# Optimization experiments

Measured on AMD Instinct MI355X. Metric: run time of the kernel, lower is better.

## Reference

```python
import jax, jax.numpy as jnp
import numpy as np

EPS = 1e-12  # torch F.normalize eps


def setup_inputs() -> dict:
    key = jax.random.key(0)
    k1, k2, k3, k4, k5 = jax.random.split(key, 5)
    N, C, H, W = 32, 512, 32, 32
    E = 1024   # expansion * dim
    G = 8      # group
    D = E // G # 128, per-group channel dim
    K = 64     # num_clusters
    x = jax.random.normal(k1, (N, C, H, W), dtype=jnp.float32)
    W1 = jax.random.normal(k2, (E, C), dtype=jnp.float32) / np.sqrt(C)
    W2 = jax.random.normal(k3, (G, E), dtype=jnp.float32) / np.sqrt(E)
    Wc = jax.random.normal(k4, (K, D), dtype=jnp.float32) / np.sqrt(D)
    centroids = jax.random.uniform(k5, (K, D), dtype=jnp.float32)
    return {"x": x, "W1": W1, "W2": W2, "Wc": Wc, "centroids": centroids}


def reference(x, W1, W2, Wc, centroids):
    # x: [N, C, H, W]; W1: [E, C]; W2: [G, E]; Wc: [K, D]; centroids: [K, D]
    N, C, H, W = x.shape
    E = W1.shape[0]
    G = W2.shape[0]
    K, D = Wc.shape
    P = H * W
    # descriptor-wise L2 normalization over channel dim
    norm = jnp.linalg.norm(x, axis=1, keepdims=True)
    x = x / jnp.maximum(norm, EPS)
    # linear1 on channels: [N, E, P]
    xe = jnp.einsum('ncp,ec->nep', x.reshape(N, C, P), W1)
    # grouped features: [N, G, D, P]
    xg = xe.reshape(N, G, D, P)
    # attention gate: sigmoid(linear2)  -> [N, G, P]
    att = jax.nn.sigmoid(jnp.einsum('nep,ge->ngp', xe, W2))
    # 1x1 conv = per-pixel matmul with cluster weights -> [N, G, K, P]
    soft_assign = jax.nn.softmax(jnp.einsum('ngdp,kd->ngkp', xg, Wc), axis=2)
    # combined per-(cluster,pixel) weight
    w = soft_assign * att[:, :, None, :]  # [N, G, K, P]
    # NetVLAD residual aggregation, algebraically decomposed to avoid the
    # giant [N,G,K,D,P] intermediate:
    #   vlad[n,k,d] = sum_{g,p} w * xg  -  centroids[k,d] * sum_{g,p} w
    agg = jnp.einsum('ngkp,ngdp->nkd', w, xg)  # [N, K, D]
    wsum = w.sum(axis=(1, 3))                  # [N, K]
    vlad = agg - wsum[:, :, None] * centroids[None]  # [N, K, D]
    return vlad.reshape(N, K * D)
```

## Files before the change

### kernel.cpp

```cpp
#include <hip/hip_runtime.h>


#define N_  32
#define C_  512
#define P_  1024
#define E_  1024
#define G_  8
#define D_  128
#define K_  64

typedef __attribute__((ext_vector_type(8))) short bf16x8;
typedef __attribute__((ext_vector_type(4))) float f32x4;

__device__ __forceinline__ unsigned short f2b(float f) {
    union { float f; unsigned u; } v; v.f = f;
    unsigned r = (v.u + 0x7FFFu + ((v.u >> 16) & 1u)) >> 16;
    return (unsigned short)r;
}
__device__ __forceinline__ float b2f(unsigned short h) {
    union { unsigned u; float f; } v; v.u = ((unsigned)h) << 16;
    return v.f;
}

__device__ __forceinline__ void gl_lds16(const void* g, void* l) {
    __builtin_amdgcn_global_load_lds(
        (const __attribute__((address_space(1))) void*)g,
        (__attribute__((address_space(3))) void*)l, 16, 0, 0);
}

__global__ __launch_bounds__(256) void k0a_convert_w1(const float* __restrict__ W1,
                                                      unsigned short* __restrict__ W1b) {
    int i = blockIdx.x * 256 + threadIdx.x;
    W1b[i] = f2b(W1[i]);
}

__global__ __launch_bounds__(256) void k0b_make_v(const float* __restrict__ W1,
                                                  const float* __restrict__ Wc,
                                                  unsigned short* __restrict__ Vb) {
    int bid = blockIdx.x;
    int ch = bid & 1, k = (bid >> 1) & 63, g = bid >> 7;
    int c = ch * 256 + threadIdx.x;
    float acc = 0.f;
    #pragma unroll 8
    for (int d = 0; d < 128; ++d) {
        acc += Wc[k * 128 + d] * W1[(g * 128 + d) * C_ + c];
    }
    Vb[(g * 64 + k) * C_ + c] = f2b(acc);
}

__global__ __launch_bounds__(256) void k1_norm_transpose(const float* __restrict__ x,
                                                         unsigned short* __restrict__ xhat_t) {
    __shared__ float rn[64];
    __shared__ float tile[64 * 65];
    int n = blockIdx.y;
    int p0 = blockIdx.x * 64;
    int t = threadIdx.x;
    int ps = t & 63, cs = t >> 6;

    float ss = 0.f;
    for (int i = 0; i < 128; ++i) {
        int c = cs * 128 + i;
        float v = x[(n * C_ + c) * P_ + p0 + ps];
        ss += v * v;
    }
    tile[t] = ss;
    __syncthreads();
    if (t < 64) {
        float s = tile[t] + tile[64 + t] + tile[128 + t] + tile[192 + t];
        rn[t] = 1.0f / fmaxf(sqrtf(s), 1e-12f);
    }
    __syncthreads();

    for (int cb = 0; cb < C_; cb += 64) {
        #pragma unroll
        for (int i = 0; i < 16; ++i) {
            int cl = (t >> 6) * 16 + i;
            tile[cl * 65 + (t & 63)] = x[(n * C_ + cb + cl) * P_ + p0 + (t & 63)];
        }
        __syncthreads();
        #pragma unroll
        for (int pr = 0; pr < 16; ++pr) {
            int ps2 = (t >> 6) * 16 + pr;
            int cl2 = t & 63;
            float v = tile[cl2 * 65 + ps2] * rn[ps2];
            xhat_t[((size_t)(n * P_ + p0 + ps2)) * C_ + cb + cl2] = f2b(v);
        }
        __syncthreads();
    }
}

__global__ __launch_bounds__(256) void k2_gemm_xe(const unsigned short* __restrict__ W1b,
                                                  const unsigned short* __restrict__ xhat_t,
                                                  unsigned short* __restrict__ xe) {
    __shared__ __align__(16) short As[128 * 32];
    __shared__ __align__(16) short Bs[128 * 32];
    int n = blockIdx.y;
    int e0 = (blockIdx.x >> 3) * 128;
    int p0 = (blockIdx.x & 7) * 128;
    int t = threadIdx.x;
    int w = t >> 6, l = t & 63, q = l >> 4, l15 = l & 15;
    int wr = w >> 1, wc = w & 1;

    f32x4 acc[4][4];
    #pragma unroll
    for (int mi = 0; mi < 4; ++mi)
        #pragma unroll
        for (int ni = 0; ni < 4; ++ni)
            acc[mi][ni] = (f32x4){0.f, 0.f, 0.f, 0.f};

    for (int ks = 0; ks < 16; ++ks) {
        int k0 = ks * 32;
        #pragma unroll
        for (int i = 0; i < 2; ++i) {
            int ch = i * 256 + t;
            int row = ch >> 2, col = (ch & 3) * 8;
            gl_lds16(&W1b[(e0 + row) * C_ + k0 + col], &As[ch * 8]);
        }
        #pragma unroll
        for (int i = 0; i < 2; ++i) {
            int ch = i * 256 + t;
            int row = ch >> 2, col = (ch & 3) * 8;
            gl_lds16(&xhat_t[((size_t)(n * P_ + p0 + row)) * C_ + k0 + col], &Bs[ch * 8]);
        }
        __syncthreads();

        bf16x8 af[4], bf[4];
        #pragma unroll
        for (int mi = 0; mi < 4; ++mi)
            af[mi] = *(const bf16x8*)&As[(wr * 64 + mi * 16 + l15) * 32 + q * 8];
        #pragma unroll
        for (int ni = 0; ni < 4; ++ni)
            bf[ni] = *(const bf16x8*)&Bs[(wc * 64 + ni * 16 + l15) * 32 + q * 8];
        #pragma unroll
        for (int mi = 0; mi < 4; ++mi)
            #pragma unroll
            for (int ni = 0; ni < 4; ++ni)
                acc[mi][ni] = __builtin_amdgcn_mfma_f32_16x16x32_bf16(af[mi], bf[ni], acc[mi][ni], 0, 0, 0);
        __syncthreads();
    }

    #pragma unroll
    for (int mi = 0; mi < 4; ++mi) {
        #pragma unroll
        for (int ni = 0; ni < 4; ++ni) {
            #pragma unroll
            for (int r = 0; r < 4; ++r) {
                int e = e0 + wr * 64 + mi * 16 + q * 4 + r;
                int p = p0 + wc * 64 + ni * 16 + l15;
                xe[((size_t)(n * E_ + e)) * P_ + p] = f2b(acc[mi][ni][r]);
            }
        }
    }
}

__global__ __launch_bounds__(256) void k3a_att_part(const unsigned short* __restrict__ xe,
                                                    const float* __restrict__ W2,
                                                    float* __restrict__ att_part) {
    int n = blockIdx.y;
    int pblk = blockIdx.x & 3, ec = blockIdx.x >> 2;
    int p = pblk * 256 + threadIdx.x;
    int e0 = ec * 64;
    float acc[8];
    #pragma unroll
    for (int g = 0; g < 8; ++g) acc[g] = 0.f;
    #pragma unroll 8
    for (int i = 0; i < 64; ++i) {
        int e = e0 + i;
        float v = b2f(xe[((size_t)(n * E_ + e)) * P_ + p]);
        #pragma unroll
        for (int g = 0; g < 8; ++g)
            acc[g] += v * W2[g * E_ + e];
    }
    #pragma unroll
    for (int g = 0; g < 8; ++g)
        att_part[(((size_t)(n * 16 + ec)) * 8 + g) * P_ + p] = acc[g];
}

__global__ __launch_bounds__(256) void k3b_att_reduce(const float* __restrict__ att_part,
                                                      float* __restrict__ att_s) {
    int idx = blockIdx.x * 256 + threadIdx.x;
    int p = idx & 1023;
    int g = (idx >> 10) & 7;
    int n = idx >> 13;
    float s = 0.f;
    #pragma unroll
    for (int ec = 0; ec < 16; ++ec)
        s += att_part[(((size_t)(n * 16 + ec)) * 8 + g) * P_ + p];
    att_s[idx] = 1.0f / (1.0f + __expf(-s));
}

__global__ __launch_bounds__(256) void k4_assign_agg(const unsigned short* __restrict__ Vb,
                                                     const unsigned short* __restrict__ xhat_t,
                                                     const unsigned short* __restrict__ xe,
                                                     const float* __restrict__ att_s,
                                                     float* __restrict__ agg_part,
                                                     float* __restrict__ wsum_part) {
    __shared__ __align__(16) short As2[64 * 32];
    __shared__ __align__(16) short Bs2[128 * 32];
    __shared__ __align__(16) short wlds[64 * 136];
    __shared__ __align__(16) short xglds[128 * 136];

    int g = blockIdx.x & 7, ph = blockIdx.x >> 3, n = blockIdx.y;
    int t = threadIdx.x;
    int w = t >> 6, l = t & 63, q = l >> 4, l15 = l & 15;

    f32x4 acc_a[4][2];
    #pragma unroll
    for (int mi = 0; mi < 4; ++mi)
        #pragma unroll
        for (int ni = 0; ni < 2; ++ni)
            acc_a[mi][ni] = (f32x4){0.f, 0.f, 0.f, 0.f};
    float wsp[16];
    #pragma unroll
    for (int j = 0; j < 16; ++j) wsp[j] = 0.f;

    for (int cc = 0; cc < 4; ++cc) {
        int p0c = ph * 512 + cc * 128;

        f32x4 acc_s[4][2];
        #pragma unroll
        for (int mi = 0; mi < 4; ++mi)
            #pragma unroll
            for (int ni = 0; ni < 2; ++ni)
                acc_s[mi][ni] = (f32x4){0.f, 0.f, 0.f, 0.f};

        for (int ks = 0; ks < 16; ++ks) {
            int k0 = ks * 32;
            {
                int row = t >> 2, col = (t & 3) * 8;
                gl_lds16(&Vb[(g * 64 + row) * C_ + k0 + col], &As2[t * 8]);
            }
            #pragma unroll
            for (int i = 0; i < 2; ++i) {
                int ch = i * 256 + t;
                int row = ch >> 2, col = (ch & 3) * 8;
                gl_lds16(&xhat_t[((size_t)(n * P_ + p0c + row)) * C_ + k0 + col], &Bs2[ch * 8]);
            }
            __syncthreads();
            bf16x8 af[4], bf2[2];
            #pragma unroll
            for (int mi = 0; mi < 4; ++mi)
                af[mi] = *(const bf16x8*)&As2[(mi * 16 + l15) * 32 + q * 8];
            #pragma unroll
            for (int ni = 0; ni < 2; ++ni)
                bf2[ni] = *(const bf16x8*)&Bs2[(w * 32 + ni * 16 + l15) * 32 + q * 8];
            #pragma unroll
            for (int mi = 0; mi < 4; ++mi)
                #pragma unroll
                for (int ni = 0; ni < 2; ++ni)
                    acc_s[mi][ni] = __builtin_amdgcn_mfma_f32_16x16x32_bf16(af[mi], bf2[ni], acc_s[mi][ni], 0, 0, 0);
            __syncthreads();
        }

        #pragma unroll
        for (int ni = 0; ni < 2; ++ni) {
            float m = -1e30f;
            #pragma unroll
            for (int mi = 0; mi < 4; ++mi)
                #pragma unroll
                for (int r = 0; r < 4; ++r)
                    m = fmaxf(m, acc_s[mi][ni][r]);
            m = fmaxf(m, __shfl_xor(m, 16));
            m = fmaxf(m, __shfl_xor(m, 32));
            float s = 0.f;
            #pragma unroll
            for (int mi = 0; mi < 4; ++mi)
                #pragma unroll
                for (int r = 0; r < 4; ++r) {
                    float e = __expf(acc_s[mi][ni][r] - m);
                    acc_s[mi][ni][r] = e;
                    s += e;
                }
            s += __shfl_xor(s, 16);
            s += __shfl_xor(s, 32);

            int pcol = p0c + w * 32 + ni * 16 + l15;
            float av = att_s[(((size_t)(n * G_ + g)) * P_) + pcol];
            float scale = av / s;

            #pragma unroll
            for (int mi = 0; mi < 4; ++mi)
                #pragma unroll
                for (int r = 0; r < 4; ++r) {
                    float wv = acc_s[mi][ni][r] * scale;
                    wsp[mi * 4 + r] += wv;
                    wlds[(mi * 16 + q * 4 + r) * 136 + (w * 32 + ni * 16 + l15)] = (short)f2b(wv);
                }
        }

        #pragma unroll
        for (int i = 0; i < 8; ++i) {
            int ch = i * 256 + t;
            int row = ch / 17, col = (ch % 17) * 8;
            gl_lds16(&xe[((size_t)(n * E_ + g * 128 + row)) * P_ + p0c + col], &xglds[ch * 8]);
        }
        if (t < 128) {
            int ch = 2048 + t;
            int row = ch / 17, col = (ch % 17) * 8;
            gl_lds16(&xe[((size_t)(n * E_ + g * 128 + row)) * P_ + p0c + col], &xglds[ch * 8]);
        }
        __syncthreads();

        #pragma unroll
        for (int pk = 0; pk < 4; ++pk) {
            bf16x8 a2[4], b2[2];
            #pragma unroll
            for (int mi = 0; mi < 4; ++mi)
                a2[mi] = *(const bf16x8*)&wlds[(mi * 16 + l15) * 136 + pk * 32 + q * 8];
            #pragma unroll
            for (int ni = 0; ni < 2; ++ni)
                b2[ni] = *(const bf16x8*)&xglds[(w * 32 + ni * 16 + l15) * 136 + pk * 32 + q * 8];
            #pragma unroll
            for (int mi = 0; mi < 4; ++mi)
                #pragma unroll
                for (int ni = 0; ni < 2; ++ni)
                    acc_a[mi][ni] = __builtin_amdgcn_mfma_f32_16x16x32_bf16(a2[mi], b2[ni], acc_a[mi][ni], 0, 0, 0);
        }
        __syncthreads();
    }

    size_t base = (((size_t)(n * G_ + g)) * 2 + ph) * 64;
    #pragma unroll
    for (int mi = 0; mi < 4; ++mi)
        #pragma unroll
        for (int ni = 0; ni < 2; ++ni)
            #pragma unroll
            for (int r = 0; r < 4; ++r) {
                int k = mi * 16 + q * 4 + r;
                int d = w * 32 + ni * 16 + l15;
                agg_part[(base + k) * 128 + d] = acc_a[mi][ni][r];
            }

    #pragma unroll
    for (int j = 0; j < 16; ++j) {
        float v = wsp[j];
        v += __shfl_xor(v, 1);
        v += __shfl_xor(v, 2);
        v += __shfl_xor(v, 4);
        v += __shfl_xor(v, 8);
        if (l15 == 0) {
            int k = (j >> 2) * 16 + q * 4 + (j & 3);
            wsum_part[((((size_t)(n * G_ + g)) * 2 + ph) * 4 + w) * 64 + k] = v;
        }
    }
}

__global__ __launch_bounds__(256) void k5_final(const float* __restrict__ agg_part,
                                                const float* __restrict__ wsum_part,
                                                const float* __restrict__ centroids,
                                                float* __restrict__ out) {
    int idx = blockIdx.x * 256 + threadIdx.x;
    int d = idx & 127;
    int k = (idx >> 7) & 63;
    int n = idx >> 13;
    float ws = 0.f;
    #pragma unroll
    for (int g = 0; g < 8; ++g)
        #pragma unroll
        for (int ph = 0; ph < 2; ++ph)
            #pragma unroll
            for (int w2 = 0; w2 < 4; ++w2)
                ws += wsum_part[((((size_t)(n * G_ + g)) * 2 + ph) * 4 + w2) * 64 + k];
    float agg = 0.f;
    #pragma unroll
    for (int g = 0; g < 8; ++g)
        #pragma unroll
        for (int ph = 0; ph < 2; ++ph)
            agg += agg_part[(((((size_t)(n * G_ + g)) * 2 + ph) * 64) + k) * 128 + d];
    out[idx] = agg - ws * centroids[k * 128 + d];
}

extern "C" void kernel_launch(void* const* d_in, const int* in_sizes, int n_in,
                              void* d_out, int out_size, void* d_ws, size_t ws_size,
                              hipStream_t stream) {
    const float* x         = (const float*)d_in[0];
    const float* W1        = (const float*)d_in[1];
    const float* W2        = (const float*)d_in[2];
    const float* Wc        = (const float*)d_in[3];
    const float* centroids = (const float*)d_in[4];
    float* out = (float*)d_out;

    char* ws = (char*)d_ws;
    unsigned short* W1b      = (unsigned short*)(ws + 0);
    unsigned short* Vb       = (unsigned short*)(ws + 1048576);
    unsigned short* xhat_t   = (unsigned short*)(ws + 1572864);
    unsigned short* xe       = (unsigned short*)(ws + 35127296);
    float*          att_s    = (float*)(ws + 102236160);
    float*          agg_part = (float*)(ws + 103284736);
    float*          att_part = (float*)(ws + 103284736);
    float*          wsum_part= (float*)(ws + 120061952);

    hipLaunchKernelGGL(k0a_convert_w1, dim3(2048), dim3(256), 0, stream, W1, W1b);
    hipLaunchKernelGGL(k0b_make_v,     dim3(1024), dim3(256), 0, stream, W1, Wc, Vb);
    hipLaunchKernelGGL(k1_norm_transpose, dim3(16, 32), dim3(256), 0, stream, x, xhat_t);
    hipLaunchKernelGGL(k2_gemm_xe,     dim3(64, 32), dim3(256), 0, stream, W1b, xhat_t, xe);
    hipLaunchKernelGGL(k3a_att_part,   dim3(64, 32), dim3(256), 0, stream, xe, W2, att_part);
    hipLaunchKernelGGL(k3b_att_reduce, dim3(1024), dim3(256), 0, stream, att_part, att_s);
    hipLaunchKernelGGL(k4_assign_agg,  dim3(16, 32), dim3(256), 0, stream, Vb, xhat_t, xe,
                       att_s, agg_part, wsum_part);
    hipLaunchKernelGGL(k5_final,       dim3(1024), dim3(256), 0, stream,
                       agg_part, wsum_part, centroids, out);
}
```

Before: 262.7 us.

## Fuse weight prep into norm kernel, vectorize attention partials, alias k4 LDS buffers

Merges the W1 bf16 conversion and the V=Wc·W1 precompute into the normalization kernel as extra blocks, which removes two launches. The normalization kernel now reads x once into a 64KB bf16 LDS stage and writes xhat_t with 16-byte vector stores, where it previously re-read x from global memory. The attention-partial kernel processes 4 pixels per thread with vector loads and stores. k4 overlaps its GEMM staging buffers with the xg buffer to cut LDS usage. The large LDS footprint in k1 may reduce occupancy, and x is rounded to bf16 before normalization, which adds a second rounding step.

```diff
diff --git a/kernel.cpp b/kernel.cpp
--- a/kernel.cpp
+++ b/kernel.cpp
@@ -28,64 +28,59 @@
         (__attribute__((address_space(3))) void*)l, 16, 0, 0);
 }
 
-__global__ __launch_bounds__(256) void k0a_convert_w1(const float* __restrict__ W1,
-                                                      unsigned short* __restrict__ W1b) {
-    int i = blockIdx.x * 256 + threadIdx.x;
-    W1b[i] = f2b(W1[i]);
-}
-
-__global__ __launch_bounds__(256) void k0b_make_v(const float* __restrict__ W1,
-                                                  const float* __restrict__ Wc,
-                                                  unsigned short* __restrict__ Vb) {
-    int bid = blockIdx.x;
-    int ch = bid & 1, k = (bid >> 1) & 63, g = bid >> 7;
-    int c = ch * 256 + threadIdx.x;
-    float acc = 0.f;
-    #pragma unroll 8
-    for (int d = 0; d < 128; ++d) {
-        acc += Wc[k * 128 + d] * W1[(g * 128 + d) * C_ + c];
-    }
-    Vb[(g * 64 + k) * C_ + c] = f2b(acc);
-}
-
-__global__ __launch_bounds__(256) void k1_norm_transpose(const float* __restrict__ x,
-                                                         unsigned short* __restrict__ xhat_t) {
+__global__ __launch_bounds__(256) void k1_norm_prep(const float* __restrict__ x,
+                                                    const float* __restrict__ W1,
+                                                    const float* __restrict__ Wc,
+                                                    unsigned short* __restrict__ xhat_t,
+                                                    unsigned short* __restrict__ W1b,
+                                                    unsigned short* __restrict__ Vb) {
+    __shared__ short xc[128 * 256];
+    __shared__ float red[256];
     __shared__ float rn[64];
-    __shared__ float tile[64 * 65];
+    int t = threadIdx.x;
+
+    if (blockIdx.x >= 16) {
+        int bid = (blockIdx.x - 16) * 32 + blockIdx.y;
+        int i0 = bid * 512 + t;
+        W1b[i0]       = f2b(W1[i0]);
+        W1b[i0 + 256] = f2b(W1[i0 + 256]);
+        int ch = bid & 1, k = (bid >> 1) & 63, g = bid >> 7;
+        int c = ch * 256 + t;
+        float acc = 0.f;
+        #pragma unroll 8
+        for (int d = 0; d < 128; ++d)
+            acc += Wc[k * 128 + d] * W1[(g * 128 + d) * C_ + c];
+        Vb[(g * 64 + k) * C_ + c] = f2b(acc);
+        return;
+    }
+
     int n = blockIdx.y;
     int p0 = blockIdx.x * 64;
-    int t = threadIdx.x;
     int ps = t & 63, cs = t >> 6;
 
     float ss = 0.f;
     for (int i = 0; i < 128; ++i) {
-        int c = cs * 128 + i;
-        float v = x[(n * C_ + c) * P_ + p0 + ps];
+        float v = x[((size_t)(n * C_ + cs * 128 + i)) * P_ + p0 + ps];
         ss += v * v;
-    }
-    tile[t] = ss;
+        xc[i * 256 + t] = (short)f2b(v);
+    }
+    red[t] = ss;
     __syncthreads();
     if (t < 64) {
-        float s = tile[t] + tile[64 + t] + tile[128 + t] + tile[192 + t];
+        float s = red[t] + red[64 + t] + red[128 + t] + red[192 + t];
         rn[t] = 1.0f / fmaxf(sqrtf(s), 1e-12f);
     }
     __syncthreads();
 
-    for (int cb = 0; cb < C_; cb += 64) {
-        #pragma unroll
-        for (int i = 0; i < 16; ++i) {
-            int cl = (t >> 6) * 16 + i;
-            tile[cl * 65 + (t & 63)] = x[(n * C_ + cb + cl) * P_ + p0 + (t & 63)];
-        }
-        __syncthreads();
-        #pragma unroll
-        for (int pr = 0; pr < 16; ++pr) {
-            int ps2 = (t >> 6) * 16 + pr;
-            int cl2 = t & 63;
-            float v = tile[cl2 * 65 + ps2] * rn[ps2];
-            xhat_t[((size_t)(n * P_ + p0 + ps2)) * C_ + cb + cl2] = f2b(v);
-        }
-        __syncthreads();
+    float r = rn[ps];
+    size_t base = ((size_t)(n * P_ + p0 + ps)) * C_ + cs * 128;
+    #pragma unroll
+    for (int jj = 0; jj < 16; ++jj) {
+        bf16x8 o;
+        #pragma unroll
+        for (int j = 0; j < 8; ++j)
+            o[j] = (short)f2b(b2f((unsigned short)xc[(jj * 8 + j) * 256 + t]) * r);
+        *(bf16x8*)&xhat_t[base + jj * 8] = o;
     }
 }
 
@@ -157,23 +152,24 @@
                                                     const float* __restrict__ W2,
                                                     float* __restrict__ att_part) {
     int n = blockIdx.y;
-    int pblk = blockIdx.x & 3, ec = blockIdx.x >> 2;
-    int p = pblk * 256 + threadIdx.x;
+    int ec = blockIdx.x;
+    int t = threadIdx.x;
     int e0 = ec * 64;
-    float acc[8];
-    #pragma unroll
-    for (int g = 0; g < 8; ++g) acc[g] = 0.f;
-    #pragma unroll 8
+    f32x4 acc[8];
+    #pragma unroll
+    for (int g = 0; g < 8; ++g) acc[g] = (f32x4){0.f, 0.f, 0.f, 0.f};
+    #pragma unroll 4
     for (int i = 0; i < 64; ++i) {
         int e = e0 + i;
-        float v = b2f(xe[((size_t)(n * E_ + e)) * P_ + p]);
+        ushort4 v4 = *(const ushort4*)&xe[((size_t)(n * E_ + e)) * P_ + t * 4];
+        f32x4 vf = {b2f(v4.x), b2f(v4.y), b2f(v4.z), b2f(v4.w)};
         #pragma unroll
         for (int g = 0; g < 8; ++g)
-            acc[g] += v * W2[g * E_ + e];
+            acc[g] += vf * W2[g * E_ + e];
     }
     #pragma unroll
     for (int g = 0; g < 8; ++g)
-        att_part[(((size_t)(n * 16 + ec)) * 8 + g) * P_ + p] = acc[g];
+        *(f32x4*)&att_part[(((size_t)(n * 16 + ec)) * 8 + g) * P_ + t * 4] = acc[g];
 }
 
 __global__ __launch_bounds__(256) void k3b_att_reduce(const float* __restrict__ att_part,
@@ -195,10 +191,11 @@
                                                      const float* __restrict__ att_s,
                                                      float* __restrict__ agg_part,
                                                      float* __restrict__ wsum_part) {
-    __shared__ __align__(16) short As2[64 * 32];
-    __shared__ __align__(16) short Bs2[128 * 32];
-    __shared__ __align__(16) short wlds[64 * 136];
-    __shared__ __align__(16) short xglds[128 * 136];
+    __shared__ __align__(16) char smem[34816 + 17408];
+    short* xglds = (short*)smem;
+    short* As2   = (short*)smem;
+    short* Bs2   = (short*)(smem + 4096);
+    short* wlds  = (short*)(smem + 34816);
 
     int g = blockIdx.x & 7, ph = blockIdx.x >> 3, n = blockIdx.y;
     int t = threadIdx.x;
@@ -386,15 +383,14 @@
     unsigned short* xhat_t   = (unsigned short*)(ws + 1572864);
     unsigned short* xe       = (unsigned short*)(ws + 35127296);
     float*          att_s    = (float*)(ws + 102236160);
+    float*          att_part = (float*)(ws + 103284736);
     float*          agg_part = (float*)(ws + 103284736);
-    float*          att_part = (float*)(ws + 103284736);
     float*          wsum_part= (float*)(ws + 120061952);
 
-    hipLaunchKernelGGL(k0a_convert_w1, dim3(2048), dim3(256), 0, stream, W1, W1b);
-    hipLaunchKernelGGL(k0b_make_v,     dim3(1024), dim3(256), 0, stream, W1, Wc, Vb);
-    hipLaunchKernelGGL(k1_norm_transpose, dim3(16, 32), dim3(256), 0, stream, x, xhat_t);
+    hipLaunchKernelGGL(k1_norm_prep,   dim3(48, 32), dim3(256), 0, stream,
+                       x, W1, Wc, xhat_t, W1b, Vb);
     hipLaunchKernelGGL(k2_gemm_xe,     dim3(64, 32), dim3(256), 0, stream, W1b, xhat_t, xe);
-    hipLaunchKernelGGL(k3a_att_part,   dim3(64, 32), dim3(256), 0, stream, xe, W2, att_part);
+    hipLaunchKernelGGL(k3a_att_part,   dim3(16, 32), dim3(256), 0, stream, xe, W2, att_part);
     hipLaunchKernelGGL(k3b_att_reduce, dim3(1024), dim3(256), 0, stream, att_part, att_s);
     hipLaunchKernelGGL(k4_assign_agg,  dim3(16, 32), dim3(256), 0, stream, Vb, xhat_t, xe,
                        att_s, agg_part, wsum_part);
```

After: 262.7 us. About the same (+0.0%).
